# Kernel tuning notes

Measured on AMD Instinct MI355X. Metric: run time of the kernel, lower is better.

The kernel has to match this reference:

```python
import jax, jax.numpy as jnp
import numpy as np

B, N, M = 8, 4096, 4096


def setup_inputs() -> dict:
    key = jax.random.key(0)
    ks = jax.random.split(key, 8)
    return {
        "x_aligned": jax.random.normal(ks[0], (B, N, 3), dtype=jnp.float32),
        "y": jax.random.normal(ks[1], (B, M, 3), dtype=jnp.float32),
        "R": jax.random.normal(ks[2], (B, 3, 3), dtype=jnp.float32),
        "S": jax.random.normal(ks[3], (B, 3), dtype=jnp.float32),
        "t": jax.random.normal(ks[4], (B, 3, 1), dtype=jnp.float32),
        "R_gt": jax.random.normal(ks[5], (B, 3, 3), dtype=jnp.float32),
        "S_gt": jax.random.normal(ks[6], (B, 3), dtype=jnp.float32),
        "t_gt": jax.random.normal(ks[7], (B, 3), dtype=jnp.float32),
    }


def chamfer_distance(x, y):
    # x: [B,N,3], y: [B,M,3]; bidirectional mean squared NN distance
    xn = jnp.sum(x * x, axis=-1)                      # [B,N]
    yn = jnp.sum(y * y, axis=-1)                      # [B,M]
    xy = jnp.einsum('bnd,bmd->bnm', x, y)             # [B,N,M]
    d2 = xn[:, :, None] + yn[:, None, :] - 2.0 * xy   # [B,N,M] squared dists
    cham_x = jnp.mean(jnp.min(d2, axis=2), axis=1)    # [B] x -> y
    cham_y = jnp.mean(jnp.min(d2, axis=1), axis=1)    # [B] y -> x
    return jnp.mean(cham_x) + jnp.mean(cham_y)        # batch mean, summed dirs


def reference(x_aligned, y, R, S, t, R_gt, S_gt, t_gt):
    t = jnp.squeeze(t)                                # [B,3]
    eye = jnp.eye(3, dtype=R.dtype)
    R_loss = jnp.einsum('bij,bkj->bik', R, R_gt) - eye  # R @ R_gt^T - I
    L_reg = (jnp.sum(R_loss * R_loss)
             + jnp.sum((S - S_gt) ** 2)
             + jnp.sum((t - t_gt) ** 2))
    L_chamfer = chamfer_distance(x_aligned, y)
    return L_reg + L_chamfer
```

## Files before the change

### kernel.cpp

```cpp
#include <hip/hip_runtime.h>

#define BB 8
#define NN 4096
#define MC 64
#define NCHUNK (NN / MC)
#define KPT 16
#define TPB 128
#define PTS_PER_BLOCK (TPB * KPT)
#define NPTS (2 * BB * NN)


typedef __attribute__((ext_vector_type(2))) float f2;

__device__ __forceinline__ f2 pk_fma(f2 a, f2 b, f2 c) {
  f2 d;
  asm("v_pk_fma_f32 %0, %1, %2, %3" : "=v"(d) : "v"(a), "v"(b), "v"(c));
  return d;
}

__global__ __launch_bounds__(TPB) void chamfer_partial(
    const float* __restrict__ X, const float* __restrict__ Y,
    unsigned int* __restrict__ nnmin, float* __restrict__ out) {
  __shared__ float4 lxy[MC / 2];
  __shared__ float4 lzw[MC / 2];
  const int tid = threadIdx.x;
  const int zb  = blockIdx.z;
  const int b   = zb & (BB - 1);
  const int dir = zb >> 3;
  const float* pts  = dir ? (Y + b * NN * 3) : (X + b * NN * 3);
  const float* refs = dir ? (X + b * NN * 3) : (Y + b * NN * 3);
  const int c = blockIdx.y;

  if (blockIdx.x == 0 && blockIdx.y == 0 && blockIdx.z == 0 && tid == 0)
    out[0] = 0.0f;

  if (tid < MC / 2) {
    const int j = c * MC + 2 * tid;
    const float a0 = refs[j * 3 + 0], a1 = refs[j * 3 + 1], a2 = refs[j * 3 + 2];
    const float b0 = refs[j * 3 + 3], b1 = refs[j * 3 + 4], b2 = refs[j * 3 + 5];
    lxy[tid] = make_float4(-2.0f * a0, -2.0f * b0, -2.0f * a1, -2.0f * b1);
    lzw[tid] = make_float4(-2.0f * a2, -2.0f * b2,
                           a0 * a0 + a1 * a1 + a2 * a2,
                           b0 * b0 + b1 * b1 + b2 * b2);
  }

  f2 px2[KPT], py2[KPT], pz2[KPT];
  float m[KPT];
  const int p0 = blockIdx.x * PTS_PER_BLOCK + tid;
#pragma unroll
  for (int k = 0; k < KPT; k++) {
    const int p = p0 + k * TPB;
    const float qx = pts[p * 3 + 0];
    const float qy = pts[p * 3 + 1];
    const float qz = pts[p * 3 + 2];
    px2[k] = (f2){qx, qx};
    py2[k] = (f2){qy, qy};
    pz2[k] = (f2){qz, qz};
    m[k] = 1e30f;
  }
  __syncthreads();

#pragma unroll 2
  for (int jp = 0; jp < MC / 2; jp++) {
    const float4 wxy = lxy[jp];
    const float4 wzw = lzw[jp];
    const f2 xp = (f2){wxy.x, wxy.y};
    const f2 yp = (f2){wxy.z, wxy.w};
    const f2 zp = (f2){wzw.x, wzw.y};
    const f2 wp = (f2){wzw.z, wzw.w};
#pragma unroll
    for (int k = 0; k < KPT; k++) {
      f2 s = pk_fma(pz2[k], zp, wp);
      s = pk_fma(py2[k], yp, s);
      s = pk_fma(px2[k], xp, s);
      m[k] = fminf(m[k], fminf(s.x, s.y));
    }
  }

#pragma unroll
  for (int k = 0; k < KPT; k++) {
    const int p = p0 + k * TPB;
    const float qx = px2[k].x, qy = py2[k].x, qz = pz2[k].x;
    const float pn = qx * qx + qy * qy + qz * qz;
    const float d2 = fmaxf(m[k] + pn, 0.0f);
    atomicMin(&nnmin[zb * NN + p], __float_as_uint(d2));
  }
}

__global__ __launch_bounds__(256) void chamfer_reduce(
    const float* __restrict__ nnmin,
    const float* __restrict__ R, const float* __restrict__ S,
    const float* __restrict__ t, const float* __restrict__ Rgt,
    const float* __restrict__ Sgt, const float* __restrict__ tgt,
    float* __restrict__ out) {
  const int tid = threadIdx.x;
  const int base = blockIdx.x * 2048;
  const float4* v = (const float4*)nnmin;
  const float4 a0 = v[(base >> 2) + tid];
  const float4 a1 = v[(base >> 2) + 256 + tid];
  float s = (a0.x + a0.y) + (a0.z + a0.w) + (a1.x + a1.y) + (a1.z + a1.w);
  for (int o = 32; o > 0; o >>= 1) s += __shfl_down(s, o);
  __shared__ float wsum[4];
  if ((tid & 63) == 0) wsum[tid >> 6] = s;
  __syncthreads();
  if (tid == 0) {
    const float bs = wsum[0] + wsum[1] + wsum[2] + wsum[3];
    atomicAdd(out, bs * (1.0f / (float)(BB * NN)));
  }

  if (blockIdx.x == 0) {
    float v2 = 0.0f;
    if (tid < 72) {
      const int b = tid / 9, ik = tid % 9, i = ik / 3, k = ik % 3;
      const float* Rb = R + b * 9;
      const float* Gb = Rgt + b * 9;
      float d = Rb[i * 3 + 0] * Gb[k * 3 + 0] +
                Rb[i * 3 + 1] * Gb[k * 3 + 1] +
                Rb[i * 3 + 2] * Gb[k * 3 + 2];
      d -= (i == k) ? 1.0f : 0.0f;
      v2 = d * d;
    } else if (tid < 96) {
      const int i = tid - 72;
      const float d = S[i] - Sgt[i];
      v2 = d * d;
    } else if (tid < 120) {
      const int i = tid - 96;
      const float d = t[i] - tgt[i];
      v2 = d * d;
    }
    for (int o = 32; o > 0; o >>= 1) v2 += __shfl_down(v2, o);
    __shared__ float rsum[4];
    if ((tid & 63) == 0) rsum[tid >> 6] = v2;
    __syncthreads();
    if (tid == 0) atomicAdd(out, rsum[0] + rsum[1] + rsum[2] + rsum[3]);
  }
}

extern "C" void kernel_launch(void* const* d_in, const int* in_sizes, int n_in,
                              void* d_out, int out_size, void* d_ws, size_t ws_size,
                              hipStream_t stream) {
  const float* X   = (const float*)d_in[0];
  const float* Y   = (const float*)d_in[1];
  const float* R   = (const float*)d_in[2];
  const float* S   = (const float*)d_in[3];
  const float* t   = (const float*)d_in[4];
  const float* Rgt = (const float*)d_in[5];
  const float* Sgt = (const float*)d_in[6];
  const float* tgt = (const float*)d_in[7];

  unsigned int* nnmin = (unsigned int*)d_ws;
  float* out = (float*)d_out;

  hipMemsetAsync(nnmin, 0x7F, NPTS * sizeof(unsigned int), stream);

  dim3 gA(NN / PTS_PER_BLOCK, NCHUNK, 2 * BB);
  chamfer_partial<<<gA, TPB, 0, stream>>>(X, Y, nnmin, out);

  chamfer_reduce<<<NPTS / 2048, 256, 0, stream>>>((const float*)nnmin,
                                                  R, S, t, Rgt, Sgt, tgt, out);
}
```

Before: 99.15 us.

## Pack two query points per register pair and broadcast refs via op_sel

Query points are now packed two per f2 register instead of being duplicated across both lanes. The packed FMAs use op_sel/op_sel_hi to broadcast each reference lane, and the min compares are kept per lane. This halves the query register footprint, and KPT drops from 16 to 8 with a launch-bounds occupancy hint of 8. The aim is more waves in flight, paid for with twice as many blocks, which means more LDS reference loads and redundant chunk setup per point.

```diff
diff --git a/kernel.cpp b/kernel.cpp
--- a/kernel.cpp
+++ b/kernel.cpp
@@ -4,7 +4,7 @@
 #define NN 4096
 #define MC 64
 #define NCHUNK (NN / MC)
-#define KPT 16
+#define KPT 8
 #define TPB 128
 #define PTS_PER_BLOCK (TPB * KPT)
 #define NPTS (2 * BB * NN)
@@ -12,13 +12,32 @@
 
 typedef __attribute__((ext_vector_type(2))) float f2;
 
-__device__ __forceinline__ f2 pk_fma(f2 a, f2 b, f2 c) {
+__device__ __forceinline__ f2 pk_fma_lo_bc(f2 a, f2 b, f2 c) {
   f2 d;
-  asm("v_pk_fma_f32 %0, %1, %2, %3" : "=v"(d) : "v"(a), "v"(b), "v"(c));
+  asm("v_pk_fma_f32 %0, %1, %2, %3 op_sel:[0,0,0] op_sel_hi:[1,0,0]"
+      : "=v"(d) : "v"(a), "v"(b), "v"(c));
+  return d;
+}
+__device__ __forceinline__ f2 pk_fma_lo_b(f2 a, f2 b, f2 c) {
+  f2 d;
+  asm("v_pk_fma_f32 %0, %1, %2, %3 op_sel:[0,0,0] op_sel_hi:[1,0,1]"
+      : "=v"(d) : "v"(a), "v"(b), "v"(c));
+  return d;
+}
+__device__ __forceinline__ f2 pk_fma_hi_bc(f2 a, f2 b, f2 c) {
+  f2 d;
+  asm("v_pk_fma_f32 %0, %1, %2, %3 op_sel:[0,1,1] op_sel_hi:[1,1,1]"
+      : "=v"(d) : "v"(a), "v"(b), "v"(c));
+  return d;
+}
+__device__ __forceinline__ f2 pk_fma_hi_b(f2 a, f2 b, f2 c) {
+  f2 d;
+  asm("v_pk_fma_f32 %0, %1, %2, %3 op_sel:[0,1,0] op_sel_hi:[1,1,1]"
+      : "=v"(d) : "v"(a), "v"(b), "v"(c));
   return d;
 }
 
-__global__ __launch_bounds__(TPB) void chamfer_partial(
+__global__ __launch_bounds__(TPB, 8) void chamfer_partial(
     const float* __restrict__ X, const float* __restrict__ Y,
     unsigned int* __restrict__ nnmin, float* __restrict__ out) {
   __shared__ float4 lxy[MC / 2];
@@ -44,19 +63,16 @@
                            b0 * b0 + b1 * b1 + b2 * b2);
   }
 
-  f2 px2[KPT], py2[KPT], pz2[KPT];
-  float m[KPT];
+  f2 qx[KPT / 2], qy[KPT / 2], qz[KPT / 2], m2[KPT / 2];
   const int p0 = blockIdx.x * PTS_PER_BLOCK + tid;
 #pragma unroll
-  for (int k = 0; k < KPT; k++) {
-    const int p = p0 + k * TPB;
-    const float qx = pts[p * 3 + 0];
-    const float qy = pts[p * 3 + 1];
-    const float qz = pts[p * 3 + 2];
-    px2[k] = (f2){qx, qx};
-    py2[k] = (f2){qy, qy};
-    pz2[k] = (f2){qz, qz};
-    m[k] = 1e30f;
+  for (int i = 0; i < KPT / 2; i++) {
+    const int pa = p0 + (2 * i) * TPB;
+    const int pb = p0 + (2 * i + 1) * TPB;
+    qx[i] = (f2){pts[pa * 3 + 0], pts[pb * 3 + 0]};
+    qy[i] = (f2){pts[pa * 3 + 1], pts[pb * 3 + 1]};
+    qz[i] = (f2){pts[pa * 3 + 2], pts[pb * 3 + 2]};
+    m2[i] = (f2){1e30f, 1e30f};
   }
   __syncthreads();
 
@@ -64,26 +80,33 @@
   for (int jp = 0; jp < MC / 2; jp++) {
     const float4 wxy = lxy[jp];
     const float4 wzw = lzw[jp];
-    const f2 xp = (f2){wxy.x, wxy.y};
-    const f2 yp = (f2){wxy.z, wxy.w};
-    const f2 zp = (f2){wzw.x, wzw.y};
-    const f2 wp = (f2){wzw.z, wzw.w};
+    const f2 Px = (f2){wxy.x, wxy.y};
+    const f2 Py = (f2){wxy.z, wxy.w};
+    const f2 Pz = (f2){wzw.x, wzw.y};
+    const f2 Pw = (f2){wzw.z, wzw.w};
 #pragma unroll
-    for (int k = 0; k < KPT; k++) {
-      f2 s = pk_fma(pz2[k], zp, wp);
-      s = pk_fma(py2[k], yp, s);
-      s = pk_fma(px2[k], xp, s);
-      m[k] = fminf(m[k], fminf(s.x, s.y));
+    for (int i = 0; i < KPT / 2; i++) {
+      f2 s = pk_fma_lo_bc(qz[i], Pz, Pw);
+      s = pk_fma_lo_b(qy[i], Py, s);
+      s = pk_fma_lo_b(qx[i], Px, s);
+      f2 t = pk_fma_hi_bc(qz[i], Pz, Pw);
+      t = pk_fma_hi_b(qy[i], Py, t);
+      t = pk_fma_hi_b(qx[i], Px, t);
+      m2[i].x = fminf(m2[i].x, fminf(s.x, t.x));
+      m2[i].y = fminf(m2[i].y, fminf(s.y, t.y));
     }
   }
 
 #pragma unroll
-  for (int k = 0; k < KPT; k++) {
-    const int p = p0 + k * TPB;
-    const float qx = px2[k].x, qy = py2[k].x, qz = pz2[k].x;
-    const float pn = qx * qx + qy * qy + qz * qz;
-    const float d2 = fmaxf(m[k] + pn, 0.0f);
-    atomicMin(&nnmin[zb * NN + p], __float_as_uint(d2));
+  for (int i = 0; i < KPT / 2; i++) {
+    const int pa = p0 + (2 * i) * TPB;
+    const int pb = p0 + (2 * i + 1) * TPB;
+    const float na = qx[i].x * qx[i].x + qy[i].x * qy[i].x + qz[i].x * qz[i].x;
+    const float nb = qx[i].y * qx[i].y + qy[i].y * qy[i].y + qz[i].y * qz[i].y;
+    const float da = fmaxf(m2[i].x + na, 0.0f);
+    const float db = fmaxf(m2[i].y + nb, 0.0f);
+    atomicMin(&nnmin[zb * NN + pa], __float_as_uint(da));
+    atomicMin(&nnmin[zb * NN + pb], __float_as_uint(db));
   }
 }
 
```

Measured after the change: 108.2 us. 9.1% more time.
